# Kernel tuning notes

Measured on AMD Instinct MI355X. Metric: run time of the kernel, lower is better.

## Reference

```python
import jax, jax.numpy as jnp
import numpy as np
import math

B, S, D, H, DFF = 16, 1024, 512, 8, 2048
DH = D // H
EPS = 1e-5


def setup_inputs() -> dict:
    key = jax.random.key(0)
    ks = jax.random.split(key, 16)
    sc = 0.02
    inp = {
        "x": jax.random.normal(ks[0], (B, S, D), dtype=jnp.float32),
        "mask": jnp.zeros((B, 1, 1, S), dtype=jnp.float32),
        # attention projections (stored as [in, out])
        "wq": jax.random.normal(ks[1], (D, D), jnp.float32) * sc,
        "bq": jnp.zeros((D,), jnp.float32),
        "wk": jax.random.normal(ks[2], (D, D), jnp.float32) * sc,
        "bk": jnp.zeros((D,), jnp.float32),
        "wv": jax.random.normal(ks[3], (D, D), jnp.float32) * sc,
        "bv": jnp.zeros((D,), jnp.float32),
        "wo": jax.random.normal(ks[4], (D, D), jnp.float32) * sc,
        "bo": jnp.zeros((D,), jnp.float32),
        # FFN
        "w1": jax.random.normal(ks[5], (D, DFF), jnp.float32) * sc,
        "b1": jnp.zeros((DFF,), jnp.float32),
        "w2": jax.random.normal(ks[6], (DFF, D), jnp.float32) * sc,
        "b2": jnp.zeros((D,), jnp.float32),
        # LayerNorms over the full [S, D] slab (normalized_shape=[S, D])
        "ln1_w": jnp.ones((S, D), jnp.float32),
        "ln1_b": jnp.zeros((S, D), jnp.float32),
        "ln2_w": jnp.ones((S, D), jnp.float32),
        "ln2_b": jnp.zeros((S, D), jnp.float32),
    }
    return inp


def _layernorm_2d(x, w, b):
    # torch nn.LayerNorm([S, D]): normalize jointly over last two dims
    m = jnp.mean(x, axis=(-2, -1), keepdims=True)
    v = jnp.mean(jnp.square(x - m), axis=(-2, -1), keepdims=True)
    return (x - m) * jax.lax.rsqrt(v + EPS) * w + b


def _encoder_layer(x, mask, wq, bq, wk, bk, wv, bv, wo, bo,
                   w1, b1, w2, b2, ln1_w, ln1_b, ln2_w, ln2_b):
    # --- multi-head attention ---
    def heads(t):  # [B,S,D] -> [B,H,S,DH]
        return t.reshape(B, S, H, DH).transpose(0, 2, 1, 3)

    q = heads(x @ wq + bq)
    k = heads(x @ wk + bk)
    v = heads(x @ wv + bv)

    logits = jnp.einsum("bhqd,bhkd->bhqk", q, k) / math.sqrt(DH)
    logits = logits + mask * -1e9
    attn = jax.nn.softmax(logits, axis=-1)          # [B,H,S,S]
    ctx = jnp.einsum("bhqk,bhkd->bhqd", attn, v)    # [B,H,S,DH]
    ctx = ctx.transpose(0, 2, 1, 3).reshape(B, S, D)
    attn_out = ctx @ wo + bo

    out1 = _layernorm_2d(x + attn_out, ln1_w, ln1_b)

    # --- FFN ---
    ffn = jax.nn.relu(out1 @ w1 + b1) @ w2 + b2
    out2 = _layernorm_2d(out1 + ffn, ln2_w, ln2_b)
    return out2


def reference(x, mask, wq, bq, wk, bk, wv, bv, wo, bo,
              w1, b1, w2, b2, ln1_w, ln1_b, ln2_w, ln2_b):
    return _encoder_layer(x, mask, wq, bq, wk, bk, wv, bv, wo, bo,
                          w1, b1, w2, b2, ln1_w, ln1_b, ln2_w, ln2_b)
```

## Files before the change

### kernel.cpp

```cpp
#include <hip/hip_runtime.h>
#include <stdint.h>

#define B_   16
#define S_   1024
#define D_   512
#define H_   8
#define DH_  64
#define DFF_ 2048
#define M_   (B_*S_)
#define SD_  (S_*D_)

typedef unsigned short u16;
typedef unsigned int u32;
typedef __attribute__((ext_vector_type(4))) unsigned short u16x4;
typedef __attribute__((ext_vector_type(8))) short bf16x8;
typedef __attribute__((ext_vector_type(4))) float f32x4;
typedef __attribute__((ext_vector_type(16))) float f32x16;

#define LOG2E 1.4426950408889634f

__device__ __forceinline__ u16 f2bf(float f) {
  union { float f; uint32_t u; } x{f};
  uint32_t r = x.u + 0x7fffu + ((x.u >> 16) & 1u);
  return (u16)(r >> 16);
}

__device__ __forceinline__ float bf2f(u16 v) {
  union { uint32_t u; float f; } x{(uint32_t)v << 16};
  return x.f;
}

__device__ __forceinline__ u32 pk2(float lo, float hi) {
  union { float f; u32 u; } a{lo}, b{hi};
  return __builtin_amdgcn_perm(b.u, a.u, 0x07060302u);
}

__device__ __forceinline__ float exp2fast(float x) {
#if __has_builtin(__builtin_amdgcn_exp2f)
  return __builtin_amdgcn_exp2f(x);
#else
  return exp2f(x);
#endif
}

__device__ __forceinline__ void gload16(const u16* g, u16* l) {
  __builtin_amdgcn_global_load_lds(
      (const __attribute__((address_space(1))) uint32_t*)g,
      (__attribute__((address_space(3))) uint32_t*)l, 16, 0, 0);
}

__device__ __forceinline__ int swz3(int r) { return (r & 7) ^ ((r >> 3) & 7); }

__global__ __launch_bounds__(256) void prep_kernel(
    const float* __restrict__ x, u16* __restrict__ xb,
    const float* __restrict__ wq, const float* __restrict__ wk,
    const float* __restrict__ wv, const float* __restrict__ wo,
    const float* __restrict__ w1, const float* __restrict__ w2,
    u16* __restrict__ wqkvT, u16* __restrict__ woT,
    u16* __restrict__ w1T, u16* __restrict__ w2T) {
  int bid = blockIdx.x, tid = threadIdx.x;
  if (bid < 8192) {
    int i = bid * 256 + tid;
    f32x4 v = ((const f32x4*)x)[i];
    u16x4 o = { f2bf(v[0]), f2bf(v[1]), f2bf(v[2]), f2bf(v[3]) };
    ((u16x4*)xb)[i] = o;
    return;
  }
  bid -= 8192;
  const float* W; u16* WT; int K, N, bx, by;
  if (bid < 1024) {
    int which = bid >> 8;
    W  = (which == 0) ? wq : (which == 1) ? wk : (which == 2) ? wv : wo;
    WT = (which == 3) ? woT : (wqkvT + (size_t)which * 512 * 512);
    K = 512; N = 512;
    int r = bid & 255; bx = r & 15; by = r >> 4;
  } else if (bid < 2048) {
    int r = bid - 1024; W = w1; WT = w1T; K = 512; N = 2048;
    bx = r & 63; by = r >> 6;
  } else {
    int r = bid - 2048; W = w2; WT = w2T; K = 2048; N = 512;
    bx = r & 15; by = r >> 4;
  }
  __shared__ float t[32][33];
  int n0 = bx * 32, k0 = by * 32;
  int tx = tid & 31, ty = tid >> 5;
  #pragma unroll
  for (int i = 0; i < 4; i++)
    t[ty + 8*i][tx] = W[(size_t)(k0 + ty + 8*i) * N + n0 + tx];
  __syncthreads();
  #pragma unroll
  for (int i = 0; i < 4; i++)
    WT[(size_t)(n0 + ty + 8*i) * K + k0 + tx] = f2bf(t[tx][ty + 8*i]);
}

template<int MODE, bool RELU>
__global__ __launch_bounds__(512, 2) void gemm256_kernel(
    const u16* __restrict__ A, const u16* __restrict__ WT,
    const float* __restrict__ bias0, const float* __restrict__ bias1,
    const float* __restrict__ bias2,
    u16* __restrict__ out0, u16* __restrict__ out1, u16* __restrict__ out2,
    int K, int ostride, int nx, int ypg) {
  __shared__ u16 lA[2][16384];
  __shared__ u16 lB[2][16384];
  int tid = threadIdx.x, lane = tid & 63;
  int wid = tid >> 6, wm = wid >> 2, wn = wid & 3;
  int l16 = lane & 15, kg4 = lane >> 4;

  int d = blockIdx.x;
  int c = d & 7, j = d >> 3;
  int x = j % nx, y = c * ypg + j / nx;
  int m0 = y * 256, n0 = x * 256;

  const u16* agp = A  + (size_t)m0 * K;
  const u16* bgp = WT + (size_t)n0 * K;
  int srow = tid >> 3, sslot = tid & 7;

  f32x4 z = {0.f, 0.f, 0.f, 0.f};
  f32x4 acc[8][4];
  #pragma unroll
  for (int mg = 0; mg < 8; mg++)
    #pragma unroll
    for (int ni = 0; ni < 4; ni++) acc[mg][ni] = z;

#define STAGE256(buf, kt) do { \
    _Pragma("unroll") \
    for (int h = 0; h < 2; h++) \
      _Pragma("unroll") \
      for (int i = 0; i < 2; i++) { \
        int r_ = h*128 + i*64 + srow; \
        int gc_ = (kt) + ((sslot ^ swz3(r_)) << 3); \
        gload16(agp + (size_t)r_ * K + gc_, &lA[buf][h*8192 + (i*512 + tid)*8]); \
        gload16(bgp + (size_t)r_ * K + gc_, &lB[buf][h*8192 + (i*512 + tid)*8]); \
      } \
  } while (0)

  int nk = K / 64;
  int cur = 0;
  STAGE256(0, 0);

  for (int t = 0; t < nk; t++) {
    __syncthreads();
    if (t + 1 < nk) STAGE256(cur ^ 1, (t + 1) * 64);
    bf16x8 bfv[4][2];
    #pragma unroll
    for (int ni = 0; ni < 4; ni++)
      #pragma unroll
      for (int kf = 0; kf < 2; kf++) {
        int row = wn*64 + ni*16 + l16;
        int slot = (kf*4 + kg4) ^ swz3(row);
        bfv[ni][kf] = *(const bf16x8*)&lB[cur][row*64 + slot*8];
      }
    #pragma unroll
    for (int p = 0; p < 4; p++) {
      bf16x8 af[2][2];
      #pragma unroll
      for (int mi = 0; mi < 2; mi++)
        #pragma unroll
        for (int kf = 0; kf < 2; kf++) {
          int row = wm*128 + p*32 + mi*16 + l16;
          int slot = (kf*4 + kg4) ^ swz3(row);
          af[mi][kf] = *(const bf16x8*)&lA[cur][row*64 + slot*8];
        }
      __builtin_amdgcn_s_setprio(1);
      #pragma unroll
      for (int kf = 0; kf < 2; kf++)
        #pragma unroll
        for (int mi = 0; mi < 2; mi++)
          #pragma unroll
          for (int ni = 0; ni < 4; ni++)
            acc[p*2 + mi][ni] = __builtin_amdgcn_mfma_f32_16x16x32_bf16(
                af[mi][kf], bfv[ni][kf], acc[p*2 + mi][ni], 0, 0, 0);
      __builtin_amdgcn_s_setprio(0);
      __builtin_amdgcn_sched_barrier(0);
    }
    cur ^= 1;
  }
#undef STAGE256

  int segbase = n0 + wn*64;
  int seg = segbase >> 9;
  const float* bp = (MODE == 2) ? (seg == 0 ? bias0 : (seg == 1 ? bias1 : bias2)) : bias0;
  u16* op = (MODE == 2) ? (seg == 0 ? out0 : (seg == 1 ? out1 : out2)) : out0;
  float aeff = (MODE == 2 && seg == 0) ? 0.125f * LOG2E : 1.0f;

  #pragma unroll
  for (int mg = 0; mg < 8; mg++)
    #pragma unroll
    for (int ni = 0; ni < 4; ni++) {
      int col = segbase + ni*16 + l16;
      int ocol = (MODE == 2) ? (col & 511) : col;
      float bv = bp[ocol];
      #pragma unroll
      for (int r = 0; r < 4; r++) {
        int row = m0 + wm*128 + mg*16 + kg4*4 + r;
        float v = (acc[mg][ni][r] + bv) * aeff;
        if (RELU) v = fmaxf(v, 0.f);
        op[(size_t)row * ostride + ocol] = f2bf(v);
      }
    }
}

template<int MODE, bool RELU, bool RESB>
__global__ __launch_bounds__(256) void gemm_kernel(
    const u16* __restrict__ A, const u16* __restrict__ WT,
    const float* __restrict__ bias0, const float* __restrict__ res,
    const u16* __restrict__ resB,
    u16* __restrict__ out0,
    float* __restrict__ partOut, int K, int N, int nx, int ypg) {
  __shared__ u16 lA[2][128 * 32];
  __shared__ u16 lB[2][128 * 32];
  __shared__ float lred[8];
  int tid = threadIdx.x;
  int lane = tid & 63, wid = tid >> 6;
  int wr = wid >> 1, wc = wid & 1;
  int lrow = lane & 15, kg = lane >> 4;

  int dd = blockIdx.x;
  int cc = dd & 7, jj = dd >> 3;
  int bx = jj % nx, by = cc * ypg + jj / nx;
  int m0 = by * 128, n0 = bx * 128;

  int r0 = tid >> 2, c0 = (tid & 3) * 8;
  const u16* agp = A  + (size_t)m0 * K;
  const u16* bgp = WT + (size_t)n0 * K;

  f32x4 z = {0.f, 0.f, 0.f, 0.f};
  f32x4 acc[4][4];
  #pragma unroll
  for (int mi = 0; mi < 4; mi++)
    #pragma unroll
    for (int ni = 0; ni < 4; ni++) acc[mi][ni] = z;

#define STAGE_G(buf, kt) do { \
    gload16(agp + (size_t)r0 * K + (kt) + c0,        &lA[buf][tid * 8]); \
    gload16(agp + (size_t)(r0 + 64) * K + (kt) + c0, &lA[buf][2048 + tid * 8]); \
    gload16(bgp + (size_t)r0 * K + (kt) + c0,        &lB[buf][tid * 8]); \
    gload16(bgp + (size_t)(r0 + 64) * K + (kt) + c0, &lB[buf][2048 + tid * 8]); \
  } while (0)

  STAGE_G(0, 0);

  int nk = K / 32;
  int cur = 0;
  for (int t = 0; t < nk; t++) {
    __syncthreads();
    if (t + 1 < nk) STAGE_G(cur ^ 1, (t + 1) * 32);
    bf16x8 af[4], bfv[4];
    #pragma unroll
    for (int mi = 0; mi < 4; mi++)
      af[mi] = *(const bf16x8*)&lA[cur][(wr*64 + mi*16 + lrow) * 32 + kg*8];
    #pragma unroll
    for (int ni = 0; ni < 4; ni++)
      bfv[ni] = *(const bf16x8*)&lB[cur][(wc*64 + ni*16 + lrow) * 32 + kg*8];
    __builtin_amdgcn_s_setprio(1);
    #pragma unroll
    for (int mi = 0; mi < 4; mi++)
      #pragma unroll
      for (int ni = 0; ni < 4; ni++)
        acc[mi][ni] = __builtin_amdgcn_mfma_f32_16x16x32_bf16(af[mi], bfv[ni], acc[mi][ni], 0, 0, 0);
    __builtin_amdgcn_s_setprio(0);
    cur ^= 1;
  }
#undef STAGE_G

  float s_acc = 0.f, q_acc = 0.f;
  #pragma unroll
  for (int mi = 0; mi < 4; mi++)
    #pragma unroll
    for (int ni = 0; ni < 4; ni++) {
      int col = n0 + wc*64 + ni*16 + lrow;
      float bv = bias0[col];
      #pragma unroll
      for (int r = 0; r < 4; r++) {
        int row = m0 + wr*64 + mi*16 + kg*4 + r;
        float v = acc[mi][ni][r] + bv;
        if (RELU) v = fmaxf(v, 0.f);
        size_t off = (size_t)row * N + col;
        if (MODE == 1) {
          float rv = RESB ? bf2f(resB[off]) : res[off];
          float tv = v + rv;
          out0[off] = f2bf(tv);
          s_acc += tv;
          q_acc += tv * tv;
        } else {
          out0[off] = f2bf(v);
        }
      }
    }

  if (MODE == 1) {
    #pragma unroll
    for (int dsh = 1; dsh < 64; dsh <<= 1) {
      s_acc += __shfl_xor(s_acc, dsh);
      q_acc += __shfl_xor(q_acc, dsh);
    }
    if (lane == 0) { lred[wid*2] = s_acc; lred[wid*2+1] = q_acc; }
    __syncthreads();
    if (tid == 0) {
      int batch = by >> 3;
      int pidx = batch*32 + (by & 7)*nx + bx;
      partOut[pidx*2]   = lred[0]+lred[2]+lred[4]+lred[6];
      partOut[pidx*2+1] = lred[1]+lred[3]+lred[5]+lred[7];
    }
  }
}

__global__ __launch_bounds__(256) void attn_kernel(
    const u16* __restrict__ Q, const u16* __restrict__ Km,
    const u16* __restrict__ Vm, const float* __restrict__ mask,
    u16* __restrict__ ctx) {
  __shared__ u16 lK[2][4096];
  __shared__ u16 lV[2][4096];
  __shared__ float lBias[1024];
  int tid = threadIdx.x, lane = tid & 63, wid = tid >> 6;
  int la = lane & 31, hi = lane >> 5;
  int wg = blockIdx.x;
  int xcd = wg & 7, idx = wg >> 3;
  int bh = xcd * 16 + (idx & 15);
  int qt = idx >> 4;
  int b = bh >> 3, h = bh & 7;

  const u16* qp = Q + (size_t)(b*S_ + qt*128 + wid*32 + la) * D_ + h*DH_ + hi*8;
  bf16x8 qf[4];
  #pragma unroll
  for (int c = 0; c < 4; c++) qf[c] = *(const bf16x8*)(qp + c*16);

  int krow = tid >> 3;
  int kcol = 8 * (tid & 7);
  int kc0 = kcol ^ (swz3(krow) << 3);
  int kc1 = kcol ^ (swz3(krow + 32) << 3);
  int va = tid & 7, vp = tid >> 3;
  const u16* kbase = Km + ((size_t)b*S_) * D_ + h*DH_;
  const u16* vbase = Vm + ((size_t)b*S_) * D_ + h*DH_ + 8*va;

#define STAGE_K(buf, tt) do { \
    const u16* kt_ = kbase + (size_t)(tt)*64*D_; \
    gload16(kt_ + (size_t)krow*D_ + kc0,        &lK[buf][tid*8]); \
    gload16(kt_ + (size_t)(krow+32)*D_ + kc1,   &lK[buf][2048 + tid*8]); \
  } while (0)
#define LOAD_V(tt) do { \
    const u16* vt_ = vbase + (size_t)((tt)*64 + 2*vp) * D_; \
    nv0 = *(const bf16x8*)vt_; nv1 = *(const bf16x8*)(vt_ + D_); \
  } while (0)
#define WRITE_V(buf) do { \
    u32* lVd_ = (u32*)lV[buf]; \
    _Pragma("unroll") \
    for (int jv = 0; jv < 8; jv++) { \
      int row_ = 8*va + jv; \
      u32 pv_ = (u32)(u16)nv0[jv] | ((u32)(u16)nv1[jv] << 16); \
      lVd_[row_*32 + (vp ^ (swz3(row_) << 2))] = pv_; \
    } \
  } while (0)

  {
    f32x4 mv = ((const f32x4*)(mask + (size_t)b*S_))[tid];
    f32x4 bv;
    #pragma unroll
    for (int jj = 0; jj < 4; jj++) bv[jj] = mv[jj] * (-1.0e9f * LOG2E);
    ((f32x4*)lBias)[tid] = bv;
  }

  bf16x8 nv0, nv1;
  STAGE_K(0, 0);
  LOAD_V(0);
  WRITE_V(0);
  __syncthreads();

  f32x16 oc0, oc1;
  #pragma unroll
  for (int i = 0; i < 16; i++) { oc0[i] = 0.f; oc1[i] = 0.f; }
  float lsum = 0.f;
  int cur = 0;
  int swk0 = swz3(la) << 2, swk1 = swz3(la + 32) << 2;

  for (int t = 0; t < S_/64; t++) {
    if (t + 1 < S_/64) { STAGE_K(cur ^ 1, t + 1); LOAD_V(t + 1); }

    f32x16 s0, s1;
    #pragma unroll
    for (int rq = 0; rq < 4; rq++) {
      f32x4 bb0 = *(const f32x4*)&lBias[t*64 + rq*8 + hi*4];
      f32x4 bb1 = *(const f32x4*)&lBias[t*64 + 32 + rq*8 + hi*4];
      #pragma unroll
      for (int jj = 0; jj < 4; jj++) { s0[rq*4+jj] = bb0[jj]; s1[rq*4+jj] = bb1[jj]; }
    }
    __builtin_amdgcn_s_setprio(1);
    #pragma unroll
    for (int c = 0; c < 4; c++) {
      int dwb = c*8 + hi*4;
      bf16x8 kf0 = *(const bf16x8*)&lK[cur][la*64 + ((dwb ^ swk0) << 1)];
      bf16x8 kf1 = *(const bf16x8*)&lK[cur][(la+32)*64 + ((dwb ^ swk1) << 1)];
      s0 = __builtin_amdgcn_mfma_f32_32x32x16_bf16(kf0, qf[c], s0, 0, 0, 0);
      s1 = __builtin_amdgcn_mfma_f32_32x32x16_bf16(kf1, qf[c], s1, 0, 0, 0);
    }
    __builtin_amdgcn_s_setprio(0);
    float rs = 0.f;
    #pragma unroll
    for (int i = 0; i < 16; i++) { float e = exp2fast(s0[i]); s0[i] = e; rs += e; }
    #pragma unroll
    for (int i = 0; i < 16; i++) { float e = exp2fast(s1[i]); s1[i] = e; rs += e; }
    lsum += rs;
    __builtin_amdgcn_s_setprio(1);
    #pragma unroll
    for (int cc = 0; cc < 4; cc++) {
      const int base = 8 * (cc & 1);
      float pv[8];
      #pragma unroll
      for (int k = 0; k < 8; k++) pv[k] = (cc < 2) ? s0[base + k] : s1[base + k];
      u32 a0 = pk2(pv[0], pv[1]);
      u32 a1 = pk2(pv[2], pv[3]);
      u32 b0 = pk2(pv[4], pv[5]);
      u32 b1 = pk2(pv[6], pv[7]);
      u32 sd0 = hi ? a0 : b0, sd1 = hi ? a1 : b1;
      u32 x0 = (u32)__shfl_xor((int)sd0, 32);
      u32 x1 = (u32)__shfl_xor((int)sd1, 32);
      union { u32 u[4]; bf16x8 v; } pf;
      pf.u[0] = hi ? x0 : a0;
      pf.u[1] = hi ? x1 : a1;
      pf.u[2] = hi ? b0 : x0;
      pf.u[3] = hi ? b1 : x1;
      #pragma unroll
      for (int vb = 0; vb < 2; vb++) {
        int row = vb*32 + la;
        int dwv = (cc*8 + hi*4) ^ (swz3(row) << 2);
        bf16x8 vf = *(const bf16x8*)&lV[cur][row*64 + (dwv << 1)];
        if (vb == 0) oc0 = __builtin_amdgcn_mfma_f32_32x32x16_bf16(pf.v, vf, oc0, 0, 0, 0);
        else         oc1 = __builtin_amdgcn_mfma_f32_32x32x16_bf16(pf.v, vf, oc1, 0, 0, 0);
      }
    }
    __builtin_amdgcn_s_setprio(0);
    if (t + 1 < S_/64) {
      WRITE_V(cur ^ 1);
      __syncthreads();
      cur ^= 1;
    }
  }
#undef STAGE_K
#undef LOAD_V
#undef WRITE_V
  lsum += __shfl_xor(lsum, 32);
  float linv = 1.f / lsum;
  #pragma unroll
  for (int r = 0; r < 16; r++) {
    int qr = (r&3) + 8*(r>>2) + 4*hi;
    float lr = __shfl(linv, qr);
    size_t rowoff = (size_t)(b*S_ + qt*128 + wid*32 + qr) * D_ + h*DH_;
    ctx[rowoff + la]      = f2bf(oc0[r] * lr);
    ctx[rowoff + 32 + la] = f2bf(oc1[r] * lr);
  }
}

template<bool WB, bool WF>
__global__ __launch_bounds__(256) void ln_apply_kernel(
    const u16* __restrict__ r, const float* __restrict__ part,
    const float* __restrict__ w, const float* __restrict__ bb,
    float* __restrict__ outF, u16* __restrict__ outB) {
  int b = blockIdx.y, c = blockIdx.x, tid = threadIdx.x;
  float s = 0.f, q = 0.f;
  for (int i = 0; i < 32; i++) { s += part[(b*32+i)*2]; q += part[(b*32+i)*2+1]; }
  const float inv = 1.f / (float)SD_;
  float mean = s * inv;
  float var = q * inv - mean * mean;
  float rs = rsqrtf(var + 1e-5f);
  size_t base = (size_t)b * SD_;
  #pragma unroll
  for (int i = 0; i < 8; i++) {
    int li4 = c*2048 + i*256 + tid;
    u16x4 rv = ((const u16x4*)(r + base))[li4];
    f32x4 wv = ((const f32x4*)w)[li4];
    f32x4 bv = ((const f32x4*)bb)[li4];
    f32x4 ov;
    #pragma unroll
    for (int jj = 0; jj < 4; jj++) ov[jj] = (bf2f(rv[jj]) - mean) * rs * wv[jj] + bv[jj];
    if (WF) ((f32x4*)(outF + base))[li4] = ov;
    if (WB) {
      u16x4 ub = { f2bf(ov[0]), f2bf(ov[1]), f2bf(ov[2]), f2bf(ov[3]) };
      ((u16x4*)(outB + base))[li4] = ub;
    }
  }
}

extern "C" void kernel_launch(void* const* d_in, const int* in_sizes, int n_in,
                              void* d_out, int out_size, void* d_ws, size_t ws_size,
                              hipStream_t stream) {
  (void)in_sizes; (void)n_in; (void)out_size; (void)ws_size;
  const float* x    = (const float*)d_in[0];
  const float* mask = (const float*)d_in[1];
  const float* wq = (const float*)d_in[2];
  const float* bq = (const float*)d_in[3];
  const float* wk = (const float*)d_in[4];
  const float* bk = (const float*)d_in[5];
  const float* wv = (const float*)d_in[6];
  const float* bv = (const float*)d_in[7];
  const float* wo = (const float*)d_in[8];
  const float* bo = (const float*)d_in[9];
  const float* w1 = (const float*)d_in[10];
  const float* b1 = (const float*)d_in[11];
  const float* w2 = (const float*)d_in[12];
  const float* b2 = (const float*)d_in[13];
  const float* ln1w = (const float*)d_in[14];
  const float* ln1b = (const float*)d_in[15];
  const float* ln2w = (const float*)d_in[16];
  const float* ln2b = (const float*)d_in[17];
  float* out = (float*)d_out;

  char* ws = (char*)d_ws;
  const size_t MB = 1ull << 20;
  u16*   xb    = (u16*)(ws + 0);
  u16*   Qb    = (u16*)(ws + 16*MB);
  u16*   Kb    = (u16*)(ws + 32*MB);
  u16*   Vb    = (u16*)(ws + 48*MB);
  u16*   ctxb  = (u16*)(ws + 64*MB);
  u16*   res1b = (u16*)(ws + 80*MB);
  u16*   out1b = (u16*)(ws + 0);
  u16*   ffn1  = (u16*)(ws + 16*MB);
  u16*   res2b = (u16*)(ws + 112*MB);
  float* part  = (float*)(ws + 144*MB);
  u16*   wqkvT = (u16*)(ws + 145*MB);
  u16*   woT   = (u16*)(ws + 147*MB);
  u16*   w1T   = (u16*)(ws + 148*MB);
  u16*   w2T   = (u16*)(ws + 150*MB);

  prep_kernel<<<11264, 256, 0, stream>>>(
      x, xb, wq, wk, wv, wo, w1, w2, wqkvT, woT, w1T, w2T);

  gemm256_kernel<2,false><<<384, 512, 0, stream>>>(
      xb, wqkvT, bq, bk, bv, Qb, Kb, Vb, 512, 512, 6, 8);

  attn_kernel<<<1024, 256, 0, stream>>>(Qb, Kb, Vb, mask, ctxb);

  gemm_kernel<1,false,false><<<512, 256, 0, stream>>>(
      ctxb, woT, bo, x, nullptr, res1b, part, 512, 512, 4, 16);

  ln_apply_kernel<true,false><<<dim3(64,16), 256, 0, stream>>>(
      res1b, part, ln1w, ln1b, nullptr, out1b);

  gemm256_kernel<0,true><<<512, 512, 0, stream>>>(
      out1b, w1T, b1, nullptr, nullptr, ffn1, nullptr, nullptr, 512, 2048, 8, 8);

  gemm_kernel<1,false,true><<<512, 256, 0, stream>>>(
      ffn1, w2T, b2, nullptr, out1b, res2b, part, 2048, 512, 4, 16);

  ln_apply_kernel<false,true><<<dim3(64,16), 256, 0, stream>>>(
      res2b, part, ln2w, ln2b, out, nullptr);
}
```

Baseline: 247.9 us.

## Software-pipeline attention loop: overlap next tile QK^T with current softmax-PV

Restructures the attention inner loop so the QK^T MFMA for tile t+1 is issued before the softmax and PV MFMAs of tile t. Score accumulators are double-registered (sA/sB) and the loop is unrolled by two. K and V staging is shifted so each LDS buffer is refilled one step ahead of use. This aims to hide the exp and pack latency behind independent matrix work, at the cost of extra registers (two more f32x16 accumulators) that may lower occupancy or cause spills.

```diff
diff --git a/kernel.cpp b/kernel.cpp
--- a/kernel.cpp
+++ b/kernel.cpp
@@ -9,6 +9,7 @@
 #define DFF_ 2048
 #define M_   (B_*S_)
 #define SD_  (S_*D_)
+#define NT_  16
 
 typedef unsigned short u16;
 typedef unsigned int u32;
@@ -360,84 +361,107 @@
     ((f32x4*)lBias)[tid] = bv;
   }
 
+  int swk0 = swz3(la) << 2, swk1 = swz3(la + 32) << 2;
+  f32x16 oc0, oc1;
+  #pragma unroll
+  for (int i = 0; i < 16; i++) { oc0[i] = 0.f; oc1[i] = 0.f; }
+  float lsum = 0.f;
+
+#define QKT(d0, d1, tt) do { \
+    _Pragma("unroll") \
+    for (int rq = 0; rq < 4; rq++) { \
+      f32x4 bb0 = *(const f32x4*)&lBias[(tt)*64 + rq*8 + hi*4]; \
+      f32x4 bb1 = *(const f32x4*)&lBias[(tt)*64 + 32 + rq*8 + hi*4]; \
+      _Pragma("unroll") \
+      for (int jj = 0; jj < 4; jj++) { d0[rq*4+jj] = bb0[jj]; d1[rq*4+jj] = bb1[jj]; } \
+    } \
+    { const u16* lkb_ = lK[(tt)&1]; \
+      __builtin_amdgcn_s_setprio(1); \
+      _Pragma("unroll") \
+      for (int c_ = 0; c_ < 4; c_++) { \
+        int dwb_ = c_*8 + hi*4; \
+        bf16x8 kf0_ = *(const bf16x8*)&lkb_[la*64 + ((dwb_ ^ swk0) << 1)]; \
+        bf16x8 kf1_ = *(const bf16x8*)&lkb_[(la+32)*64 + ((dwb_ ^ swk1) << 1)]; \
+        d0 = __builtin_amdgcn_mfma_f32_32x32x16_bf16(kf0_, qf[c_], d0, 0, 0, 0); \
+        d1 = __builtin_amdgcn_mfma_f32_32x32x16_bf16(kf1_, qf[c_], d1, 0, 0, 0); \
+      } \
+      __builtin_amdgcn_s_setprio(0); } \
+  } while (0)
+
+#define SOFTPV(s0v, s1v, tt) do { \
+    float rs_ = 0.f; \
+    _Pragma("unroll") \
+    for (int i_ = 0; i_ < 16; i_++) { float e_ = exp2fast(s0v[i_]); s0v[i_] = e_; rs_ += e_; } \
+    _Pragma("unroll") \
+    for (int i_ = 0; i_ < 16; i_++) { float e_ = exp2fast(s1v[i_]); s1v[i_] = e_; rs_ += e_; } \
+    lsum += rs_; \
+    { const u16* lvb_ = lV[(tt)&1]; \
+      __builtin_amdgcn_s_setprio(1); \
+      _Pragma("unroll") \
+      for (int cc_ = 0; cc_ < 4; cc_++) { \
+        const int base_ = 8 * (cc_ & 1); \
+        float pv_[8]; \
+        _Pragma("unroll") \
+        for (int k_ = 0; k_ < 8; k_++) pv_[k_] = (cc_ < 2) ? s0v[base_ + k_] : s1v[base_ + k_]; \
+        u32 a0_ = pk2(pv_[0], pv_[1]); \
+        u32 a1_ = pk2(pv_[2], pv_[3]); \
+        u32 b0_ = pk2(pv_[4], pv_[5]); \
+        u32 b1_ = pk2(pv_[6], pv_[7]); \
+        u32 sd0_ = hi ? a0_ : b0_, sd1_ = hi ? a1_ : b1_; \
+        u32 x0_ = (u32)__shfl_xor((int)sd0_, 32); \
+        u32 x1_ = (u32)__shfl_xor((int)sd1_, 32); \
+        union { u32 u[4]; bf16x8 v; } pf_; \
+        pf_.u[0] = hi ? x0_ : a0_; \
+        pf_.u[1] = hi ? x1_ : a1_; \
+        pf_.u[2] = hi ? b0_ : x0_; \
+        pf_.u[3] = hi ? b1_ : x1_; \
+        _Pragma("unroll") \
+        for (int vb_ = 0; vb_ < 2; vb_++) { \
+          int row_ = vb_*32 + la; \
+          int dwv_ = (cc_*8 + hi*4) ^ (swz3(row_) << 2); \
+          bf16x8 vf_ = *(const bf16x8*)&lvb_[row_*64 + (dwv_ << 1)]; \
+          if (vb_ == 0) oc0 = __builtin_amdgcn_mfma_f32_32x32x16_bf16(pf_.v, vf_, oc0, 0, 0, 0); \
+          else          oc1 = __builtin_amdgcn_mfma_f32_32x32x16_bf16(pf_.v, vf_, oc1, 0, 0, 0); \
+        } \
+      } \
+      __builtin_amdgcn_s_setprio(0); } \
+  } while (0)
+
   bf16x8 nv0, nv1;
   STAGE_K(0, 0);
   LOAD_V(0);
   WRITE_V(0);
+  LOAD_V(1);
+  STAGE_K(1, 1);
   __syncthreads();
 
-  f32x16 oc0, oc1;
-  #pragma unroll
-  for (int i = 0; i < 16; i++) { oc0[i] = 0.f; oc1[i] = 0.f; }
-  float lsum = 0.f;
-  int cur = 0;
-  int swk0 = swz3(la) << 2, swk1 = swz3(la + 32) << 2;
-
-  for (int t = 0; t < S_/64; t++) {
-    if (t + 1 < S_/64) { STAGE_K(cur ^ 1, t + 1); LOAD_V(t + 1); }
-
-    f32x16 s0, s1;
-    #pragma unroll
-    for (int rq = 0; rq < 4; rq++) {
-      f32x4 bb0 = *(const f32x4*)&lBias[t*64 + rq*8 + hi*4];
-      f32x4 bb1 = *(const f32x4*)&lBias[t*64 + 32 + rq*8 + hi*4];
-      #pragma unroll
-      for (int jj = 0; jj < 4; jj++) { s0[rq*4+jj] = bb0[jj]; s1[rq*4+jj] = bb1[jj]; }
-    }
-    __builtin_amdgcn_s_setprio(1);
-    #pragma unroll
-    for (int c = 0; c < 4; c++) {
-      int dwb = c*8 + hi*4;
-      bf16x8 kf0 = *(const bf16x8*)&lK[cur][la*64 + ((dwb ^ swk0) << 1)];
-      bf16x8 kf1 = *(const bf16x8*)&lK[cur][(la+32)*64 + ((dwb ^ swk1) << 1)];
-      s0 = __builtin_amdgcn_mfma_f32_32x32x16_bf16(kf0, qf[c], s0, 0, 0, 0);
-      s1 = __builtin_amdgcn_mfma_f32_32x32x16_bf16(kf1, qf[c], s1, 0, 0, 0);
-    }
-    __builtin_amdgcn_s_setprio(0);
-    float rs = 0.f;
-    #pragma unroll
-    for (int i = 0; i < 16; i++) { float e = exp2fast(s0[i]); s0[i] = e; rs += e; }
-    #pragma unroll
-    for (int i = 0; i < 16; i++) { float e = exp2fast(s1[i]); s1[i] = e; rs += e; }
-    lsum += rs;
-    __builtin_amdgcn_s_setprio(1);
-    #pragma unroll
-    for (int cc = 0; cc < 4; cc++) {
-      const int base = 8 * (cc & 1);
-      float pv[8];
-      #pragma unroll
-      for (int k = 0; k < 8; k++) pv[k] = (cc < 2) ? s0[base + k] : s1[base + k];
-      u32 a0 = pk2(pv[0], pv[1]);
-      u32 a1 = pk2(pv[2], pv[3]);
-      u32 b0 = pk2(pv[4], pv[5]);
-      u32 b1 = pk2(pv[6], pv[7]);
-      u32 sd0 = hi ? a0 : b0, sd1 = hi ? a1 : b1;
-      u32 x0 = (u32)__shfl_xor((int)sd0, 32);
-      u32 x1 = (u32)__shfl_xor((int)sd1, 32);
-      union { u32 u[4]; bf16x8 v; } pf;
-      pf.u[0] = hi ? x0 : a0;
-      pf.u[1] = hi ? x1 : a1;
-      pf.u[2] = hi ? b0 : x0;
-      pf.u[3] = hi ? b1 : x1;
-      #pragma unroll
-      for (int vb = 0; vb < 2; vb++) {
-        int row = vb*32 + la;
-        int dwv = (cc*8 + hi*4) ^ (swz3(row) << 2);
-        bf16x8 vf = *(const bf16x8*)&lV[cur][row*64 + (dwv << 1)];
-        if (vb == 0) oc0 = __builtin_amdgcn_mfma_f32_32x32x16_bf16(pf.v, vf, oc0, 0, 0, 0);
-        else         oc1 = __builtin_amdgcn_mfma_f32_32x32x16_bf16(pf.v, vf, oc1, 0, 0, 0);
-      }
-    }
-    __builtin_amdgcn_s_setprio(0);
-    if (t + 1 < S_/64) {
-      WRITE_V(cur ^ 1);
+  f32x16 sA0, sA1, sB0, sB1;
+  QKT(sA0, sA1, 0);
+  __syncthreads();
+
+  for (int t = 0; t < NT_; t += 2) {
+    if (t + 2 < NT_) STAGE_K(t & 1, t + 2);
+    WRITE_V((t + 1) & 1);
+    if (t + 2 < NT_) LOAD_V(t + 2);
+    QKT(sB0, sB1, t + 1);
+    SOFTPV(sA0, sA1, t);
+    __syncthreads();
+    {
+      int u = t + 1;
+      if (u + 2 < NT_) STAGE_K(u & 1, u + 2);
+      if (u + 1 < NT_) WRITE_V((u + 1) & 1);
+      if (u + 2 < NT_) LOAD_V(u + 2);
+      if (u + 1 < NT_) QKT(sA0, sA1, u + 1);
+      SOFTPV(sB0, sB1, u);
       __syncthreads();
-      cur ^= 1;
     }
   }
 #undef STAGE_K
 #undef LOAD_V
 #undef WRITE_V
+#undef QKT
+#undef SOFTPV
+
   lsum += __shfl_xor(lsum, 32);
   float linv = 1.f / lsum;
   #pragma unroll
```

New measurement: 244.2 us, median of 2. No clear change (-1.5%).
